# Kernel tuning notes

Measured on AMD Instinct MI355X. Metric: run time of the kernel, lower is better.

The kernel has to match this reference:

```python
import jax, jax.numpy as jnp
import numpy as np

H = 768          # hidden_size
V = 32000        # vocab_size
NUM_GATES = 5    # none/dontcare/ptr/yes/no
PAD = 0          # pad_token_id


def setup_inputs() -> dict:
    key = jax.random.key(0)
    ks = jax.random.split(key, 10)
    B, S, J, Ls = 16, 512, 30, 4
    max_len = 8
    sc = 1.0 / np.sqrt(H).astype(np.float32)
    E = jax.random.normal(ks[0], (V, H), jnp.float32) * sc
    E = E.at[PAD].set(0.0)  # padding_idx row is zero
    return dict(
        input_ids=jax.random.randint(ks[1], (B, S), 0, V),
        encoder_output=jax.random.normal(ks[2], (B, S, H), jnp.float32),
        hidden=jax.random.normal(ks[3], (1, B, H), jnp.float32),
        input_masks=jnp.ones((B, S), jnp.int32),  # 1 = valid token
        slot=jax.random.randint(ks[4], (J, Ls), 0, V),
        max_len=max_len,
        E=E,
        W_ih=jax.random.normal(ks[5], (3 * H, H), jnp.float32) * sc,
        W_hh=jax.random.normal(ks[6], (3 * H, H), jnp.float32) * sc,
        b_ih=jnp.zeros((3 * H,), jnp.float32),
        b_hh=jnp.zeros((3 * H,), jnp.float32),
        W_gen=jax.random.normal(ks[7], (3 * H, 1), jnp.float32) * sc,
        b_gen=jnp.zeros((1,), jnp.float32),
        W_gate=jax.random.normal(ks[8], (H, NUM_GATES), jnp.float32) * sc,
        b_gate=jnp.zeros((NUM_GATES,), jnp.float32),
    )


def gru_step(x, h, W_ih, W_hh, b_ih, b_hh):
    # PyTorch GRUCell math
    gi = x @ W_ih.T + b_ih
    gh = h @ W_hh.T + b_hh
    ir, iz, inn = jnp.split(gi, 3, axis=-1)
    hr, hz, hn = jnp.split(gh, 3, axis=-1)
    r = jax.nn.sigmoid(ir + hr)
    z = jax.nn.sigmoid(iz + hz)
    n = jnp.tanh(inn + r * hn)
    return (1.0 - z) * n + z * h


def reference(input_ids, encoder_output, hidden, input_masks, slot, max_len,
              E, W_ih, W_hh, b_ih, b_hh, W_gen, b_gen, W_gate, b_gate):
    B, S, Hd = encoder_output.shape
    J = slot.shape[0]
    mask = input_masks != 1                         # True -> masked (pad)
    slot_e = E[slot].sum(axis=1)                    # [J, H]
    BJ = B * J
    # parallel decoding: flat index = b*J + j (matches repeat/repeat_interleave)
    w = jnp.tile(slot_e, (B, 1))                    # [BJ, H]
    h = jnp.repeat(hidden[0], J, axis=0)            # [BJ, H]
    enc = jnp.repeat(encoder_output, J, axis=0)     # [BJ, S, H]
    ids = jnp.repeat(input_ids, J, axis=0)          # [BJ, S]
    msk = jnp.repeat(mask, J, axis=0)               # [BJ, S]
    rows = jnp.arange(BJ)

    def step(carry, _):
        w, h = carry
        h = gru_step(w, h, W_ih, W_hh, b_ih, b_hh)                    # [BJ, H]
        attn_e = jnp.einsum('bsh,bh->bs', enc, h)                     # [BJ, S]
        attn_e = jnp.where(msk, -1e9, attn_e)
        attn_history = jax.nn.softmax(attn_e, axis=-1)                # [BJ, S]
        attn_vocab = jax.nn.softmax(h @ E.T, axis=-1)                 # [BJ, V]
        context = jnp.einsum('bs,bsh->bh', attn_history, enc)         # [BJ, H]
        p_gen = jax.nn.sigmoid(
            jnp.concatenate([w, h, context], -1) @ W_gen + b_gen)     # [BJ, 1]
        ptr = jnp.zeros_like(attn_vocab).at[rows[:, None], ids].add(attn_history)
        p_final = p_gen * attn_vocab + (1.0 - p_gen) * ptr            # [BJ, V]
        w_next = E[jnp.argmax(p_final, axis=-1)]                      # greedy (teacher=None)
        return (w_next, h), (p_final, context)

    (_, _), (points, contexts) = jax.lax.scan(step, (w, h), None, length=max_len)
    gate_logit = contexts[0] @ W_gate + b_gate                        # gate from step k==0
    all_points = points.transpose(1, 0, 2).reshape(B, J, max_len, V)
    all_gates = gate_logit.reshape(B, J, NUM_GATES)
    return all_points, all_gates
```

## Files before the change

kernel.cpp:

```cpp
#include <hip/hip_runtime.h>
#include <cstdint>
#include <cstddef>

#define HDIM 768
#define VOCAB 32000
#define NGATES 5
#define NJ 30
#define NB 16
#define NS 512
#define NBJ (NB*NJ)
#define G3 2304
#define PR 608
#define NBV 250

typedef _Float16 f16;
typedef _Float16 f16x8 __attribute__((ext_vector_type(8)));
typedef float f32x4 __attribute__((ext_vector_type(4)));

#define GLOBAL_AS __attribute__((address_space(1)))
#define LDS_AS    __attribute__((address_space(3)))

__global__ void k_cast(const float* __restrict__ src, f16* __restrict__ dst, int n) {
    for (int i = blockIdx.x*256 + threadIdx.x; i < n; i += gridDim.x*256)
        dst[i] = (f16)src[i];
}

__global__ void k_cast_split(const float* __restrict__ src, f16* __restrict__ hi,
                             f16* __restrict__ lo, int n) {
    for (int i = blockIdx.x*256 + threadIdx.x; i < n; i += gridDim.x*256) {
        float v = src[i];
        f16 h = (f16)v;
        hi[i] = h;
        lo[i] = (f16)(v - (float)h);
    }
}

__global__ void k_init_state(const float* __restrict__ E, const int* __restrict__ slot,
                             const float* __restrict__ hidden,
                             f16* __restrict__ w_hi, f16* __restrict__ w_lo,
                             float* __restrict__ h,
                             f16* __restrict__ h_hi, f16* __restrict__ h_lo) {
    int total = NBJ*HDIM;
    for (int i = blockIdx.x*256 + threadIdx.x; i < total; i += gridDim.x*256) {
        int hh = i % HDIM, row = i / HDIM;
        int b = row / NJ, j = row % NJ;
        float s = 0.f;
        #pragma unroll
        for (int l = 0; l < 4; ++l) s += E[(long)slot[j*4+l]*HDIM + hh];
        f16 sh = (f16)s;
        w_hi[i] = sh; w_lo[i] = (f16)(s - (float)sh);
        float hv = hidden[b*HDIM + hh];
        h[i] = hv;
        f16 hh16 = (f16)hv;
        h_hi[i] = hh16; h_lo[i] = (f16)(hv - (float)hh16);
    }
}

__launch_bounds__(256)
__global__ void k_gemm(const f16* __restrict__ Ah, const f16* __restrict__ Al,
                       const f16* __restrict__ Bh, const f16* __restrict__ Bl,
                       float* __restrict__ Cf, f16* __restrict__ Ch,
                       float* __restrict__ psum,
                       int M, long ldc, long coff, int kdim, int nspan,
                       long aBS, long bBS, long cBS) {
    __shared__ f16 a_lds[8][128][8];
    __shared__ f16 b_lds[8][128][8];
    __shared__ float sbuf[2][128];

    const int tid = threadIdx.x;
    const int z = blockIdx.z;
    const int m0 = blockIdx.x*128, n0 = blockIdx.y*128;
    const int w = tid >> 6, lane = tid & 63;
    const int wm = (w >> 1)*64, wn = (w & 1)*64;
    const int lr = lane & 15, lg = lane >> 4;

    f32x4 acc[4][4] = {};

    for (int sp = 0; sp < nspan; ++sp) {
        const f16* Ap = ((sp < 2) ? Ah : Al) + (long)z*aBS;
        const f16* Bp = ((sp == 1) ? Bl : Bh) + (long)z*bBS;
        for (int kc = 0; kc < kdim; kc += 64) {
            #pragma unroll
            for (int i = 0; i < 4; ++i) {
                const int idx = w*4 + i;
                const int c = idx >> 1;
                const int rl = (idx & 1)*64 + lane;
                const f16* ga = Ap + (long)(m0 + rl)*kdim + kc + c*8;
                const f16* gb = Bp + (long)(n0 + rl)*kdim + kc + c*8;
                __builtin_amdgcn_global_load_lds(
                    (const GLOBAL_AS unsigned int*)ga,
                    (LDS_AS unsigned int*)((char*)&a_lds[0][0][0] + idx*1024), 16, 0, 0);
                __builtin_amdgcn_global_load_lds(
                    (const GLOBAL_AS unsigned int*)gb,
                    (LDS_AS unsigned int*)((char*)&b_lds[0][0][0] + idx*1024), 16, 0, 0);
            }
            __syncthreads();
            #pragma unroll
            for (int kk = 0; kk < 2; ++kk) {
                const int c = kk*4 + lg;
                f16x8 af[4], bf[4];
                #pragma unroll
                for (int mi = 0; mi < 4; ++mi) af[mi] = *(const f16x8*)&a_lds[c][wm + mi*16 + lr][0];
                #pragma unroll
                for (int nf = 0; nf < 4; ++nf) bf[nf] = *(const f16x8*)&b_lds[c][wn + nf*16 + lr][0];
                #pragma unroll
                for (int mi = 0; mi < 4; ++mi)
                    #pragma unroll
                    for (int nf = 0; nf < 4; ++nf)
                        acc[mi][nf] = __builtin_amdgcn_mfma_f32_16x16x32_f16(af[mi], bf[nf], acc[mi][nf], 0, 0, 0);
            }
            __syncthreads();
        }
    }

    if (Ch != nullptr) {
        f16* Cb = Ch + (long)z*cBS + coff;
        #pragma unroll
        for (int mi = 0; mi < 4; ++mi)
            #pragma unroll
            for (int nf = 0; nf < 4; ++nf) {
                int col = n0 + wn + nf*16 + lr;
                int rowb = m0 + wm + mi*16 + lg*4;
                #pragma unroll
                for (int r = 0; r < 4; ++r) {
                    int row = rowb + r;
                    if (row < M) Cb[(long)row*ldc + col] = (f16)acc[mi][nf][r];
                }
            }
    } else {
        float* Cb = Cf + (long)z*cBS + coff;
        #pragma unroll
        for (int mi = 0; mi < 4; ++mi)
            #pragma unroll
            for (int nf = 0; nf < 4; ++nf) {
                int col = n0 + wn + nf*16 + lr;
                int rowb = m0 + wm + mi*16 + lg*4;
                #pragma unroll
                for (int r = 0; r < 4; ++r) {
                    int row = rowb + r;
                    if (row < M) Cb[(long)row*ldc + col] = acc[mi][nf][r];
                }
            }
    }

    if (psum != nullptr) {
        #pragma unroll
        for (int mi = 0; mi < 4; ++mi) {
            #pragma unroll
            for (int r = 0; r < 4; ++r) {
                float s = 0.f;
                #pragma unroll
                for (int nf = 0; nf < 4; ++nf) s += expf((float)(f16)acc[mi][nf][r]);
                s += __shfl_xor(s, 1); s += __shfl_xor(s, 2);
                s += __shfl_xor(s, 4); s += __shfl_xor(s, 8);
                if (lr == 0) sbuf[w & 1][wm + mi*16 + lg*4 + r] = s;
            }
        }
        __syncthreads();
        if (tid < 128)
            psum[(long)blockIdx.y*512 + m0 + tid] = sbuf[0][tid] + sbuf[1][tid];
    }
}

__global__ void k_gru_elem(const float* __restrict__ gi, const float* __restrict__ gh,
                           const float* __restrict__ bih, const float* __restrict__ bhh,
                           float* __restrict__ h, f16* __restrict__ h_hi, f16* __restrict__ h_lo) {
    int total = NBJ*HDIM;
    for (int i = blockIdx.x*256 + threadIdx.x; i < total; i += gridDim.x*256) {
        int c = i % HDIM; long row = i / HDIM;
        long base = row*G3;
        float r = gi[base + c]        + bih[c]        + gh[base + c]        + bhh[c];
        float z = gi[base + 768 + c]  + bih[768 + c]  + gh[base + 768 + c]  + bhh[768 + c];
        float hn = gh[base + 1536 + c] + bhh[1536 + c];
        float in_ = gi[base + 1536 + c] + bih[1536 + c];
        r = 1.f/(1.f + expf(-r));
        z = 1.f/(1.f + expf(-z));
        float n = tanhf(in_ + r*hn);
        float hv = (1.f - z)*n + z*h[i];
        h[i] = hv;
        f16 hh16 = (f16)hv;
        h_hi[i] = hh16; h_lo[i] = (f16)(hv - (float)hh16);
    }
}

__launch_bounds__(256)
__global__ void k_attn(const float* __restrict__ h, const float* __restrict__ enc,
                       float* __restrict__ attn_e) {
    __shared__ float h_lds[NJ][64];
    __shared__ float e_lds[64][65];
    const int b = blockIdx.x, st = blockIdx.y;
    const int s0 = st*64;
    const int tid = threadIdx.x;
    const int s = tid & 63, jg = tid >> 6;
    float acc[8] = {};
    for (int kc = 0; kc < HDIM; kc += 64) {
        for (int idx = tid; idx < NJ*64; idx += 256) {
            int j = idx >> 6, k = idx & 63;
            h_lds[j][k] = h[((long)(b*NJ + j))*HDIM + kc + k];
        }
        #pragma unroll
        for (int i = 0; i < 4; ++i) {
            int id = tid + i*256;
            int ss = id >> 4, kq = (id & 15)*4;
            float4 v = *(const float4*)&enc[((long)b*NS + s0 + ss)*HDIM + kc + kq];
            e_lds[ss][kq+0] = v.x; e_lds[ss][kq+1] = v.y;
            e_lds[ss][kq+2] = v.z; e_lds[ss][kq+3] = v.w;
        }
        __syncthreads();
        for (int k = 0; k < 64; ++k) {
            float e = e_lds[s][k];
            #pragma unroll
            for (int i = 0; i < 8; ++i) {
                int j = jg + i*4;
                if (j < NJ) acc[i] += h_lds[j][k]*e;
            }
        }
        __syncthreads();
    }
    #pragma unroll
    for (int i = 0; i < 8; ++i) {
        int j = jg + i*4;
        if (j < NJ) attn_e[((long)(b*NJ + j))*NS + s0 + s] = acc[i];
    }
}

__launch_bounds__(256)
__global__ void k_smctxpg(float* __restrict__ ae, const int* __restrict__ masks,
                          const float* __restrict__ enc,
                          const f16* __restrict__ w_hi, const f16* __restrict__ w_lo,
                          const float* __restrict__ h,
                          const float* __restrict__ Wgen, const float* __restrict__ bgen,
                          const float* __restrict__ Wgate, const float* __restrict__ bgate,
                          float* __restrict__ pgen, float* __restrict__ out_gates, int do_gate) {
    const int row = blockIdx.x, tid = threadIdx.x;
    const int b = row / NJ;
    __shared__ float red[256];
    __shared__ float ah_l[NS];
    __shared__ float ctx_l[HDIM];

    float x0 = ae[(long)row*NS + tid];
    float x1 = ae[(long)row*NS + tid + 256];
    if (masks[b*NS + tid]       != 1) x0 = -1e9f;
    if (masks[b*NS + tid + 256] != 1) x1 = -1e9f;
    red[tid] = fmaxf(x0, x1); __syncthreads();
    for (int o = 128; o > 0; o >>= 1) { if (tid < o) red[tid] = fmaxf(red[tid], red[tid+o]); __syncthreads(); }
    float m = red[0]; __syncthreads();
    float e0 = expf(x0 - m), e1 = expf(x1 - m);
    red[tid] = e0 + e1; __syncthreads();
    for (int o = 128; o > 0; o >>= 1) { if (tid < o) red[tid] += red[tid+o]; __syncthreads(); }
    float inv = 1.f/red[0];
    float p0 = e0*inv, p1 = e1*inv;
    ae[(long)row*NS + tid]       = p0;
    ae[(long)row*NS + tid + 256] = p1;
    ah_l[tid] = p0; ah_l[tid + 256] = p1;
    __syncthreads();

    const float* eb = enc + (long)b*NS*HDIM;
    float c0 = 0.f, c1 = 0.f, c2 = 0.f;
    for (int s = 0; s < NS; ++s) {
        float a = ah_l[s];
        const float* er = eb + (long)s*HDIM;
        c0 += a*er[tid]; c1 += a*er[tid + 256]; c2 += a*er[tid + 512];
    }
    ctx_l[tid] = c0; ctx_l[tid + 256] = c1; ctx_l[tid + 512] = c2;
    __syncthreads();

    float acc = 0.f;
    for (int x = tid; x < HDIM; x += 256) {
        float wv = (float)w_hi[(long)row*HDIM + x] + (float)w_lo[(long)row*HDIM + x];
        acc += wv*Wgen[x] + h[(long)row*HDIM + x]*Wgen[768 + x] + ctx_l[x]*Wgen[1536 + x];
    }
    red[tid] = acc; __syncthreads();
    for (int o = 128; o > 0; o >>= 1) { if (tid < o) red[tid] += red[tid+o]; __syncthreads(); }
    if (tid == 0) pgen[row] = 1.f/(1.f + expf(-(red[0] + bgen[0])));

    if (do_gate) {
        for (int g = 0; g < NGATES; ++g) {
            __syncthreads();
            float a = 0.f;
            for (int x = tid; x < HDIM; x += 256) a += ctx_l[x]*Wgate[x*NGATES + g];
            red[tid] = a; __syncthreads();
            for (int o = 128; o > 0; o >>= 1) { if (tid < o) red[tid] += red[tid+o]; __syncthreads(); }
            if (tid == 0) out_gates[row*NGATES + g] = red[0] + bgate[g];
        }
    }
}

__launch_bounds__(256)
__global__ void k_scale(const f16* __restrict__ l16, float* __restrict__ out,
                        long ldrow, long coff,
                        const float* __restrict__ psum, const float* __restrict__ pgen,
                        unsigned long long* __restrict__ pamax) {
    const int row = blockIdx.x, c = blockIdx.y, tid = threadIdx.x;
    __shared__ float red[256];
    float s = 0.f;
    for (int nb = tid; nb < NBV; nb += 256) s += psum[(long)nb*512 + row];
    red[tid] = s; __syncthreads();
    for (int o = 128; o > 0; o >>= 1) { if (tid < o) red[tid] += red[tid+o]; __syncthreads(); }
    const float scale = pgen[row] / red[0];

    const f16* lb = l16 + (long)row*VOCAB;
    float* ob = out + (long)row*ldrow + coff;
    const int v0 = c*4000;
    float bv = -1.f; int bi = 0x7FFFFFFF;
    for (int v = v0 + tid; v < v0 + 4000; v += 256) {
        float val = scale*expf((float)lb[v]);
        ob[v] = val;
        if (val > bv) { bv = val; bi = v; }
    }
    __shared__ float rv[256]; __shared__ int ri[256];
    rv[tid] = bv; ri[tid] = bi; __syncthreads();
    for (int o = 128; o > 0; o >>= 1) {
        if (tid < o) {
            float v2 = rv[tid+o]; int i2 = ri[tid+o];
            if (v2 > rv[tid] || (v2 == rv[tid] && i2 < ri[tid])) { rv[tid] = v2; ri[tid] = i2; }
        }
        __syncthreads();
    }
    if (tid == 0)
        pamax[(long)row*8 + c] = ((unsigned long long)__float_as_uint(rv[0]) << 32)
                               | (unsigned long long)(0xFFFFFFFFu - (unsigned)ri[0]);
}

__launch_bounds__(256)
__global__ void k_scatter(float* __restrict__ pts, long ldrow, long coff,
                          const int* __restrict__ ids, const float* __restrict__ ah,
                          const float* __restrict__ pgen,
                          const unsigned long long* __restrict__ pamax,
                          const float* __restrict__ E,
                          f16* __restrict__ w_hi, f16* __restrict__ w_lo) {
    const int row = blockIdx.x, tid = threadIdx.x;
    const int b = row / NJ;
    float* base = pts + (long)row*ldrow + coff;
    const float cp = 1.f - pgen[row];
    float sv = -1.f; int si = 0x7FFFFFFF;
    for (int ss = tid; ss < NS; ss += 256) {
        int id = ids[(long)b*NS + ss];
        float add = cp * ah[(long)row*NS + ss];
        float old = atomicAdd(base + id, add);
        float cand = old + add;
        if (cand > sv || (cand == sv && id < si)) { sv = cand; si = id; }
    }
    __shared__ float rv[256]; __shared__ int ri[256];
    rv[tid] = sv; ri[tid] = si; __syncthreads();
    for (int o = 128; o > 0; o >>= 1) {
        if (tid < o) {
            float v2 = rv[tid+o]; int i2 = ri[tid+o];
            if (v2 > rv[tid] || (v2 == rv[tid] && i2 < ri[tid])) { rv[tid] = v2; ri[tid] = i2; }
        }
        __syncthreads();
    }
    __shared__ int bidx;
    if (tid == 0) {
        float vv = rv[0]; int ii = ri[0];
        #pragma unroll
        for (int cc = 0; cc < 8; ++cc) {
            unsigned long long pk = pamax[(long)row*8 + cc];
            float pv = __uint_as_float((unsigned)(pk >> 32));
            int pi = (int)(0xFFFFFFFFu - (unsigned)(pk & 0xFFFFFFFFu));
            if (pv > vv || (pv == vv && pi < ii)) { vv = pv; ii = pi; }
        }
        bidx = ii;
    }
    __syncthreads();
    const int idx = bidx;
    for (int x = tid; x < HDIM; x += 256) {
        float ev = E[(long)idx*HDIM + x];
        f16 eh = (f16)ev;
        w_hi[(long)row*HDIM + x] = eh;
        w_lo[(long)row*HDIM + x] = (f16)(ev - (float)eh);
    }
}

extern "C" void kernel_launch(void* const* d_in, const int* in_sizes, int n_in,
                              void* d_out, int out_size, void* d_ws, size_t ws_size,
                              hipStream_t stream) {
    const int*   input_ids = (const int*)  d_in[0];
    const float* enc       = (const float*)d_in[1];
    const float* hidden    = (const float*)d_in[2];
    const int*   masks     = (const int*)  d_in[3];
    const int*   slot      = (const int*)  d_in[4];
    const float* E     = (const float*)d_in[6];
    const float* Wih   = (const float*)d_in[7];
    const float* Whh   = (const float*)d_in[8];
    const float* bih   = (const float*)d_in[9];
    const float* bhh   = (const float*)d_in[10];
    const float* Wgen  = (const float*)d_in[11];
    const float* bgen  = (const float*)d_in[12];
    const float* Wgate = (const float*)d_in[13];
    const float* bgate = (const float*)d_in[14];

    const int ml = (out_size / NBJ - NGATES) / VOCAB;
    float* out = (float*)d_out;
    float* gates_out = out + (long)NBJ*ml*VOCAB;

    char* ws = (char*)d_ws;
    auto carve = [&](size_t bytes) { char* p = ws; ws += (bytes + 255) & ~(size_t)255; return p; };
    f16*   E16   = (f16*)carve((size_t)VOCAB*HDIM*2);
    f16*   WH2   = (f16*)carve((size_t)2*G3*HDIM*2);
    f16*   WL2   = (f16*)carve((size_t)2*G3*HDIM*2);
    f16*   SH    = (f16*)carve((size_t)2*PR*HDIM*2);
    f16*   SL    = (f16*)carve((size_t)2*PR*HDIM*2);
    float* gigh  = (float*)carve((size_t)2*NBJ*G3*4);
    float* hbuf  = (float*)carve((size_t)NBJ*HDIM*4);
    float* ae    = (float*)carve((size_t)NBJ*NS*4);
    f16*   l16   = (f16*)carve((size_t)NBJ*VOCAB*2);
    float* pgen  = (float*)carve((size_t)NBJ*4);
    float* ps    = (float*)carve((size_t)NBV*512*4);
    unsigned long long* pamax = (unsigned long long*)carve((size_t)NBJ*8*8);

    f16* WihH = WH2;  f16* WihL = WL2;
    f16* wH = SH;     f16* wL = SL;
    f16* hH = SH + (size_t)PR*HDIM;
    f16* hL = SL + (size_t)PR*HDIM;
    float* gi = gigh; float* gh = gigh + (size_t)NBJ*G3;
    (void)gi; (void)gh;

    k_cast<<<8192, 256, 0, stream>>>(E, E16, VOCAB*HDIM);
    k_cast_split<<<2048, 256, 0, stream>>>(Wih, WihH, WihL, G3*HDIM);
    k_cast_split<<<2048, 256, 0, stream>>>(Whh, WH2 + (size_t)G3*HDIM, WL2 + (size_t)G3*HDIM, G3*HDIM);
    k_init_state<<<1440, 256, 0, stream>>>(E, slot, hidden, wH, wL, hbuf, hH, hL);

    const long ldrow = (long)ml*VOCAB;
    for (int t = 0; t < ml; ++t) {
        k_gemm<<<dim3(4, 18, 2), 256, 0, stream>>>(wH, wL, WihH, WihL, gigh, nullptr, nullptr,
            NBJ, (long)G3, 0, HDIM, 3, (long)PR*HDIM, (long)G3*HDIM, (long)NBJ*G3);
        k_gru_elem<<<1440, 256, 0, stream>>>(gigh, gigh + (size_t)NBJ*G3, bih, bhh, hbuf, hH, hL);
        k_attn<<<dim3(NB, 8), 256, 0, stream>>>(hbuf, enc, ae);
        k_smctxpg<<<NBJ, 256, 0, stream>>>(ae, masks, enc, wH, wL, hbuf,
                                           Wgen, bgen, Wgate, bgate,
                                           pgen, gates_out, t == 0 ? 1 : 0);
        k_gemm<<<dim3(4, NBV, 1), 256, 0, stream>>>(hH, hL, E16, nullptr, nullptr, l16, ps,
            NBJ, (long)VOCAB, 0, HDIM, 1, 0, 0, 0);
        k_scale<<<dim3(NBJ, 8), 256, 0, stream>>>(l16, out, ldrow, (long)t*VOCAB, ps, pgen, pamax);
        k_scatter<<<NBJ, 256, 0, stream>>>(out, ldrow, (long)t*VOCAB, input_ids, ae, pgen,
                                           pamax, E, wH, wL);
    }
}
```

Baseline: 3.223 ms.

## Split softmax/context/pgen kernel and batch context over slots to reuse encoder reads

The fused per-row softmax+context+pgen kernel is split into three kernels. The new context kernel processes all 30 slot rows of a batch together, so each encoder element is read once per batch rather than once per (batch, slot) row, cutting encoder traffic about 30x. The cost is two extra launches per step, a global round trip for the context vector, and a small grid (96 blocks) for the context kernel.

```diff
diff --git a/kernel.cpp b/kernel.cpp
--- a/kernel.cpp
+++ b/kernel.cpp
@@ -225,19 +225,10 @@
 }
 
 __launch_bounds__(256)
-__global__ void k_smctxpg(float* __restrict__ ae, const int* __restrict__ masks,
-                          const float* __restrict__ enc,
-                          const f16* __restrict__ w_hi, const f16* __restrict__ w_lo,
-                          const float* __restrict__ h,
-                          const float* __restrict__ Wgen, const float* __restrict__ bgen,
-                          const float* __restrict__ Wgate, const float* __restrict__ bgate,
-                          float* __restrict__ pgen, float* __restrict__ out_gates, int do_gate) {
+__global__ void k_softmax_s(float* __restrict__ ae, const int* __restrict__ masks) {
     const int row = blockIdx.x, tid = threadIdx.x;
     const int b = row / NJ;
     __shared__ float red[256];
-    __shared__ float ah_l[NS];
-    __shared__ float ctx_l[HDIM];
-
     float x0 = ae[(long)row*NS + tid];
     float x1 = ae[(long)row*NS + tid + 256];
     if (masks[b*NS + tid]       != 1) x0 = -1e9f;
@@ -249,39 +240,58 @@
     red[tid] = e0 + e1; __syncthreads();
     for (int o = 128; o > 0; o >>= 1) { if (tid < o) red[tid] += red[tid+o]; __syncthreads(); }
     float inv = 1.f/red[0];
-    float p0 = e0*inv, p1 = e1*inv;
-    ae[(long)row*NS + tid]       = p0;
-    ae[(long)row*NS + tid + 256] = p1;
-    ah_l[tid] = p0; ah_l[tid + 256] = p1;
-    __syncthreads();
-
-    const float* eb = enc + (long)b*NS*HDIM;
-    float c0 = 0.f, c1 = 0.f, c2 = 0.f;
-    for (int s = 0; s < NS; ++s) {
-        float a = ah_l[s];
-        const float* er = eb + (long)s*HDIM;
-        c0 += a*er[tid]; c1 += a*er[tid + 256]; c2 += a*er[tid + 512];
-    }
-    ctx_l[tid] = c0; ctx_l[tid + 256] = c1; ctx_l[tid + 512] = c2;
-    __syncthreads();
-
+    ae[(long)row*NS + tid]       = e0*inv;
+    ae[(long)row*NS + tid + 256] = e1*inv;
+}
+
+__launch_bounds__(256)
+__global__ void k_context(const float* __restrict__ ah, const float* __restrict__ enc,
+                          float* __restrict__ ctx) {
+    __shared__ float a_lds[NJ][64];
+    const int b = blockIdx.x, ht = blockIdx.y;
+    const int hh = ht*128 + (threadIdx.x & 127);
+    const int jg = threadIdx.x >> 7;
+    float acc[15] = {};
+    for (int sc = 0; sc < NS; sc += 64) {
+        for (int idx = threadIdx.x; idx < NJ*64; idx += 256) {
+            int j = idx >> 6, s = idx & 63;
+            a_lds[j][s] = ah[((long)(b*NJ + j))*NS + sc + s];
+        }
+        __syncthreads();
+        for (int s = 0; s < 64; ++s) {
+            float e = enc[((long)b*NS + sc + s)*HDIM + hh];
+            #pragma unroll
+            for (int i = 0; i < 15; ++i) acc[i] += a_lds[jg + i*2][s]*e;
+        }
+        __syncthreads();
+    }
+    #pragma unroll
+    for (int i = 0; i < 15; ++i) ctx[((long)(b*NJ + jg + i*2))*HDIM + hh] = acc[i];
+}
+
+__launch_bounds__(64)
+__global__ void k_pgen(const f16* __restrict__ w_hi, const f16* __restrict__ w_lo,
+                       const float* __restrict__ h,
+                       const float* __restrict__ ctx, const float* __restrict__ Wgen,
+                       const float* __restrict__ bgen, const float* __restrict__ Wgate,
+                       const float* __restrict__ bgate, float* __restrict__ pgen,
+                       float* __restrict__ out_gates, int do_gate) {
+    const int row = blockIdx.x, lane = threadIdx.x;
     float acc = 0.f;
-    for (int x = tid; x < HDIM; x += 256) {
+    for (int x = lane; x < HDIM; x += 64) {
         float wv = (float)w_hi[(long)row*HDIM + x] + (float)w_lo[(long)row*HDIM + x];
-        acc += wv*Wgen[x] + h[(long)row*HDIM + x]*Wgen[768 + x] + ctx_l[x]*Wgen[1536 + x];
-    }
-    red[tid] = acc; __syncthreads();
-    for (int o = 128; o > 0; o >>= 1) { if (tid < o) red[tid] += red[tid+o]; __syncthreads(); }
-    if (tid == 0) pgen[row] = 1.f/(1.f + expf(-(red[0] + bgen[0])));
-
+        acc += wv                          * Wgen[x];
+        acc += h[(long)row*HDIM + x]       * Wgen[768 + x];
+        acc += ctx[(long)row*HDIM + x]     * Wgen[1536 + x];
+    }
+    for (int o = 32; o > 0; o >>= 1) acc += __shfl_down(acc, o);
+    if (lane == 0) pgen[row] = 1.f/(1.f + expf(-(acc + bgen[0])));
     if (do_gate) {
         for (int g = 0; g < NGATES; ++g) {
-            __syncthreads();
             float a = 0.f;
-            for (int x = tid; x < HDIM; x += 256) a += ctx_l[x]*Wgate[x*NGATES + g];
-            red[tid] = a; __syncthreads();
-            for (int o = 128; o > 0; o >>= 1) { if (tid < o) red[tid] += red[tid+o]; __syncthreads(); }
-            if (tid == 0) out_gates[row*NGATES + g] = red[0] + bgate[g];
+            for (int x = lane; x < HDIM; x += 64) a += ctx[(long)row*HDIM + x]*Wgate[x*NGATES + g];
+            for (int o = 32; o > 0; o >>= 1) a += __shfl_down(a, o);
+            if (lane == 0) out_gates[row*NGATES + g] = a + bgate[g];
         }
     }
 }
@@ -404,6 +414,7 @@
     float* gigh  = (float*)carve((size_t)2*NBJ*G3*4);
     float* hbuf  = (float*)carve((size_t)NBJ*HDIM*4);
     float* ae    = (float*)carve((size_t)NBJ*NS*4);
+    float* ctx   = (float*)carve((size_t)NBJ*HDIM*4);
     f16*   l16   = (f16*)carve((size_t)NBJ*VOCAB*2);
     float* pgen  = (float*)carve((size_t)NBJ*4);
     float* ps    = (float*)carve((size_t)NBV*512*4);
@@ -413,8 +424,6 @@
     f16* wH = SH;     f16* wL = SL;
     f16* hH = SH + (size_t)PR*HDIM;
     f16* hL = SL + (size_t)PR*HDIM;
-    float* gi = gigh; float* gh = gigh + (size_t)NBJ*G3;
-    (void)gi; (void)gh;
 
     k_cast<<<8192, 256, 0, stream>>>(E, E16, VOCAB*HDIM);
     k_cast_split<<<2048, 256, 0, stream>>>(Wih, WihH, WihL, G3*HDIM);
@@ -427,9 +436,10 @@
             NBJ, (long)G3, 0, HDIM, 3, (long)PR*HDIM, (long)G3*HDIM, (long)NBJ*G3);
         k_gru_elem<<<1440, 256, 0, stream>>>(gigh, gigh + (size_t)NBJ*G3, bih, bhh, hbuf, hH, hL);
         k_attn<<<dim3(NB, 8), 256, 0, stream>>>(hbuf, enc, ae);
-        k_smctxpg<<<NBJ, 256, 0, stream>>>(ae, masks, enc, wH, wL, hbuf,
-                                           Wgen, bgen, Wgate, bgate,
-                                           pgen, gates_out, t == 0 ? 1 : 0);
+        k_softmax_s<<<NBJ, 256, 0, stream>>>(ae, masks);
+        k_context<<<dim3(NB, 6), 256, 0, stream>>>(ae, enc, ctx);
+        k_pgen<<<NBJ, 64, 0, stream>>>(wH, wL, hbuf, ctx, Wgen, bgen, Wgate, bgate,
+                                       pgen, gates_out, t == 0 ? 1 : 0);
         k_gemm<<<dim3(4, NBV, 1), 256, 0, stream>>>(hH, hL, E16, nullptr, nullptr, l16, ps,
             NBJ, (long)VOCAB, 0, HDIM, 1, 0, 0, 0);
         k_scale<<<dim3(NBJ, 8), 256, 0, stream>>>(l16, out, ldrow, (long)t*VOCAB, ps, pgen, pamax);
```

New measurement: 3.409 ms. +5.8%, slower.
